# Optimization experiments

Hardware: AMD Instinct MI355X
Metric: run time of the kernel (lower is better)

## Reference

```python
import jax, jax.numpy as jnp
import numpy as np

B, S, HIDDEN = 2, 2048, 2048
NUM_HEADS, NUM_KV_HEADS, HEAD_DIM = 16, 4, 128
Q_SIZE = NUM_HEADS * HEAD_DIM          # 2048
KV_SIZE = NUM_KV_HEADS * HEAD_DIM      # 512
ROPE_THETA = 10000.0
NEG = -1e30


def setup_inputs() -> dict:
    key = jax.random.key(0)
    k1, k2, k3 = jax.random.split(key, 3)
    hidden_states = jax.random.normal(k1, (B, S, HIDDEN), jnp.float32)
    w_qkv = jax.random.normal(k2, (HIDDEN, Q_SIZE + 2 * KV_SIZE), jnp.float32) / np.sqrt(HIDDEN)
    w_o = jax.random.normal(k3, (Q_SIZE, HIDDEN), jnp.float32) / np.sqrt(Q_SIZE)
    positions = jnp.broadcast_to(jnp.arange(S, dtype=jnp.int32), (B, S))
    return {"positions": positions, "hidden_states": hidden_states,
            "w_qkv": w_qkv, "w_o": w_o}


def _rope(x, positions):
    # x: [B, S, H, D], neox-style rotate-half rope over full head_dim
    d = x.shape[-1]
    inv_freq = 1.0 / (ROPE_THETA ** (jnp.arange(0, d, 2, dtype=jnp.float32) / d))
    ang = positions[..., None].astype(jnp.float32) * inv_freq      # [B, S, D/2]
    cos = jnp.cos(ang)[:, :, None, :]
    sin = jnp.sin(ang)[:, :, None, :]
    x1, x2 = jnp.split(x, 2, axis=-1)
    return jnp.concatenate([x1 * cos - x2 * sin, x2 * cos + x1 * sin], axis=-1)


def reference(positions, hidden_states, w_qkv, w_o):
    qkv = jnp.einsum('bsh,ho->bso', hidden_states, w_qkv)
    q, k, v = jnp.split(qkv, [Q_SIZE, Q_SIZE + KV_SIZE], axis=-1)
    q = q.reshape(B, S, NUM_HEADS, HEAD_DIM)
    k = k.reshape(B, S, NUM_KV_HEADS, HEAD_DIM)
    v = v.reshape(B, S, NUM_KV_HEADS, HEAD_DIM)
    q = _rope(q, positions)
    k = _rope(k, positions)
    rep = NUM_HEADS // NUM_KV_HEADS
    k = jnp.repeat(k, rep, axis=2)   # GQA expand -> [B, S, NUM_HEADS, D]
    v = jnp.repeat(v, rep, axis=2)
    scale = HEAD_DIM ** -0.5
    scores = jnp.einsum('bqhd,bkhd->bhqk', q, k) * scale   # [B, H, S, S]
    causal = jnp.tril(jnp.ones((S, S), dtype=bool))
    scores = jnp.where(causal, scores, NEG)
    probs = jax.nn.softmax(scores, axis=-1)
    attn = jnp.einsum('bhqk,bkhd->bqhd', probs, v).reshape(B, S, Q_SIZE)
    return jnp.einsum('bsq,qh->bsh', attn, w_o)
```

## Files before the change

kernel.cpp:

```cpp
#include <hip/hip_runtime.h>
#include <hip/hip_bf16.h>
#include <stdint.h>

#define BDIM 2
#define SDIM 2048
#define HID 2048
#define NH 16
#define NKV 4
#define HD 128
#define QSZ 2048
#define KVSZ 512
#define QKVW 3072
#define TOK (BDIM*SDIM)

typedef __attribute__((ext_vector_type(8))) short bf16x8;
typedef __attribute__((ext_vector_type(4))) float f32x4;
typedef __attribute__((ext_vector_type(16))) float f32x16;

__device__ __forceinline__ short f2bf(float f) {
  return (short)__bfloat16_as_ushort(__float2bfloat16(f));
}

__device__ __forceinline__ float exp2_fast(float x) {
  float r;
  asm("v_exp_f32 %0, %1" : "=v"(r) : "v"(x));
  return r;
}

__device__ __forceinline__ void gload_lds16(const void* g, void* lds) {
  __builtin_amdgcn_global_load_lds(
      (const __attribute__((address_space(1))) void*)g,
      (__attribute__((address_space(3))) void*)lds, 16, 0, 0);
}

__global__ __launch_bounds__(256) void k_cvt_bf16(const float* __restrict__ in,
                                                  short* __restrict__ out, int n) {
  int i = (blockIdx.x * 256 + threadIdx.x) * 4;
  if (i >= n) return;
  float4 v = *(const float4*)(in + i);
  short4 o; o.x = f2bf(v.x); o.y = f2bf(v.y); o.z = f2bf(v.z); o.w = f2bf(v.w);
  *(short4*)(out + i) = o;
}

__global__ __launch_bounds__(256) void k_transpose_cvt(const float* __restrict__ in,
                                                       short* __restrict__ out,
                                                       int R, int C) {
  __shared__ short tile[64][65];
  int k0 = blockIdx.y * 64;
  int n0 = blockIdx.x * 64;
  int t = threadIdx.x;
#pragma unroll
  for (int i = 0; i < 16; ++i) {
    int idx = i * 256 + t;
    int kk = idx >> 6, nn = idx & 63;
    tile[kk][nn] = f2bf(in[(size_t)(k0 + kk) * C + n0 + nn]);
  }
  __syncthreads();
#pragma unroll
  for (int i = 0; i < 16; ++i) {
    int idx = i * 256 + t;
    int nn = idx >> 6, kk = idx & 63;
    out[(size_t)(n0 + nn) * R + k0 + kk] = tile[kk][nn];
  }
}

__global__ __launch_bounds__(256) void k_gemm_bf16(const short* __restrict__ A,
                                                   const short* __restrict__ Bt,
                                                   float* __restrict__ C,
                                                   int M, int N, int K) {
  __shared__ char lds[128 * 32 * 2 * 2];
  char* As = lds;
  char* Bs = lds + 8192;
  const int tid = threadIdx.x;
  const int w = tid >> 6, l = tid & 63;
  const int lq = l & 15, g = l >> 4;
  const int m0 = blockIdx.y * 128, n0 = blockIdx.x * 128;
  const int wm = (w >> 1) * 64, wn = (w & 1) * 64;
  f32x4 acc[4][4] = {};

  const int nk = K >> 5;
  for (int kt = 0; kt < nk; ++kt) {
    const int k0 = kt * 32;
#pragma unroll
    for (int i = 0; i < 2; ++i) {
      int ch = (w + 4 * i) * 64 + l;
      int r = ch >> 2, cc = ch & 3;
      int gc = cc ^ ((r >> 1) & 3);
      gload_lds16(A + (size_t)(m0 + r) * K + k0 + gc * 8, As + (w + 4 * i) * 1024);
      gload_lds16(Bt + (size_t)(n0 + r) * K + k0 + gc * 8, Bs + (w + 4 * i) * 1024);
    }
    __syncthreads();
    bf16x8 af[4], bfr[4];
#pragma unroll
    for (int mi = 0; mi < 4; ++mi) {
      int row = wm + mi * 16 + lq;
      af[mi] = *(const bf16x8*)(As + row * 64 + ((g ^ ((row >> 1) & 3)) * 16));
    }
#pragma unroll
    for (int ni = 0; ni < 4; ++ni) {
      int row = wn + ni * 16 + lq;
      bfr[ni] = *(const bf16x8*)(Bs + row * 64 + ((g ^ ((row >> 1) & 3)) * 16));
    }
#pragma unroll
    for (int mi = 0; mi < 4; ++mi)
#pragma unroll
      for (int ni = 0; ni < 4; ++ni)
        acc[mi][ni] = __builtin_amdgcn_mfma_f32_16x16x32_bf16(af[mi], bfr[ni],
                                                              acc[mi][ni], 0, 0, 0);
    __syncthreads();
  }
#pragma unroll
  for (int mi = 0; mi < 4; ++mi)
#pragma unroll
    for (int ni = 0; ni < 4; ++ni)
#pragma unroll
      for (int r = 0; r < 4; ++r) {
        int row = m0 + wm + mi * 16 + 4 * g + r;
        int col = n0 + wn + ni * 16 + lq;
        C[(size_t)row * N + col] = acc[mi][ni][r];
      }
}

__global__ __launch_bounds__(256) void k_gemm_qkv_rope(const short* __restrict__ A,
                                                       const short* __restrict__ Bt,
                                                       const int* __restrict__ pos,
                                                       short* __restrict__ Qh,
                                                       short* __restrict__ Kh,
                                                       short* __restrict__ VT) {
  __shared__ char lds[128 * 32 * 2 * 2];
  char* As = lds;
  char* Bs = lds + 8192;
  const int tid = threadIdx.x;
  const int w = tid >> 6, l = tid & 63;
  const int lq = l & 15, g = l >> 4;
  const int m0 = blockIdx.y * 128, n0 = blockIdx.x * 128;
  const int K = HID, N = QKVW;
  f32x4 acc[2][8] = {};

  const int nk = K >> 5;
  for (int kt = 0; kt < nk; ++kt) {
    const int k0 = kt * 32;
#pragma unroll
    for (int i = 0; i < 2; ++i) {
      int ch = (w + 4 * i) * 64 + l;
      int r = ch >> 2, cc = ch & 3;
      int gc = cc ^ ((r >> 1) & 3);
      gload_lds16(A + (size_t)(m0 + r) * K + k0 + gc * 8, As + (w + 4 * i) * 1024);
      gload_lds16(Bt + (size_t)(n0 + r) * K + k0 + gc * 8, Bs + (w + 4 * i) * 1024);
    }
    __syncthreads();
    bf16x8 af[2], bfr[8];
#pragma unroll
    for (int mi = 0; mi < 2; ++mi) {
      int row = w * 32 + mi * 16 + lq;
      af[mi] = *(const bf16x8*)(As + row * 64 + ((g ^ ((row >> 1) & 3)) * 16));
    }
#pragma unroll
    for (int ni = 0; ni < 8; ++ni) {
      int row = ni * 16 + lq;
      bfr[ni] = *(const bf16x8*)(Bs + row * 64 + ((g ^ ((row >> 1) & 3)) * 16));
    }
#pragma unroll
    for (int mi = 0; mi < 2; ++mi)
#pragma unroll
      for (int ni = 0; ni < 8; ++ni)
        acc[mi][ni] = __builtin_amdgcn_mfma_f32_16x16x32_bf16(af[mi], bfr[ni],
                                                              acc[mi][ni], 0, 0, 0);
    __syncthreads();
  }

  const int hx = blockIdx.x;
  const int b = m0 >> 11;
  if (hx < 20) {
    const float qscale = 0.12751743920f;
    const float sc = (hx < 16) ? qscale : 1.0f;
    short* dst = (hx < 16) ? (Qh + (size_t)(b * NH + hx) * SDIM * HD)
                           : (Kh + (size_t)(b * NKV + (hx - 16)) * SDIM * HD);
    float invf[4];
#pragma unroll
    for (int ni = 0; ni < 4; ++ni)
      invf[ni] = expf(-(float)(ni * 16 + lq) * (9.210340371976184f / 64.0f));
#pragma unroll
    for (int mi = 0; mi < 2; ++mi)
#pragma unroll
      for (int r = 0; r < 4; ++r) {
        int row = m0 + w * 32 + mi * 16 + 4 * g + r;
        int s = row & (SDIM - 1);
        float p = (float)pos[row];
        size_t hb = (size_t)s * HD;
#pragma unroll
        for (int ni = 0; ni < 4; ++ni) {
          float sn, cs;
          sincosf(p * invf[ni], &sn, &cs);
          float x1 = acc[mi][ni][r], x2 = acc[mi][ni + 4][r];
          dst[hb + ni * 16 + lq] = f2bf((x1 * cs - x2 * sn) * sc);
          dst[hb + ni * 16 + lq + 64] = f2bf((x2 * cs + x1 * sn) * sc);
        }
      }
  } else {
    const int hv = hx - 20;
    const int s00 = (m0 & (SDIM - 1)) + w * 32;
#pragma unroll
    for (int mi = 0; mi < 2; ++mi)
#pragma unroll
      for (int ni = 0; ni < 8; ++ni) {
        int d = ni * 16 + lq;
        int s0 = s00 + mi * 16 + 4 * g;
        size_t vb = ((size_t)(b * NKV + hv) * HD + d) * SDIM + s0;
        short4 ov;
        ov.x = f2bf(acc[mi][ni][0]); ov.y = f2bf(acc[mi][ni][1]);
        ov.z = f2bf(acc[mi][ni][2]); ov.w = f2bf(acc[mi][ni][3]);
        *(short4*)(VT + vb) = ov;
      }
  }
}

__global__ __launch_bounds__(256, 3) void k_attn(const short* __restrict__ Qh,
                                                 const short* __restrict__ Kh,
                                                 const short* __restrict__ VT,
                                                 short* __restrict__ attn, int S) {
  __shared__ char lds[2][16384];
  const int tid = threadIdx.x;
  const int w = tid >> 6, l = tid & 63;
  const int l31 = l & 31, hi = l >> 5;
  const int nqc = S / 128;
  const int bid = blockIdx.x;
  const int b = bid / (NH * nqc);
  const int rem = bid % (NH * nqc);
  const int h = rem / nqc;
  const int qc = nqc - 1 - (rem % nqc);
  const int q0 = qc * 128 + w * 32;
  const int kvh = h >> 2;
  const short* Qp = Qh + (size_t)(b * NH + h) * S * HD;
  const short* Kp = Kh + (size_t)(b * NKV + kvh) * S * HD;
  const short* Vp = VT + (size_t)(b * NKV + kvh) * HD * S;

  bf16x8 qf[8];
#pragma unroll
  for (int kc = 0; kc < 8; ++kc)
    qf[kc] = *(const bf16x8*)(Qp + (size_t)(q0 + l31) * HD + kc * 16 + hi * 8);

  f32x16 o[4] = {};
  float mrun = -1e30f, lrun = 0.f;
  const int qabs = q0 + l31;
  const int ntu = qc * 4 + 4;

#define STAGE(bufi, c0_)                                                          \
  {                                                                               \
    char* Kb = lds[bufi];                                                         \
    char* Vb = lds[bufi] + 8192;                                                  \
    _Pragma("unroll")                                                             \
    for (int i = 0; i < 2; ++i) {                                                 \
      int id = (i * 4 + w) * 64 + l;                                              \
      int kr = id >> 4, c16 = id & 15;                                            \
      gload_lds16(Kp + (size_t)((c0_) + kr) * HD + ((c16 ^ (kr & 7)) * 8),        \
                  Kb + (i * 4 + w) * 1024);                                       \
      int vr = id >> 2, c4 = id & 3;                                              \
      gload_lds16(Vp + (size_t)vr * S + (c0_) + ((c4 ^ ((vr >> 1) & 3)) * 8),     \
                  Vb + (i * 4 + w) * 1024);                                       \
    }                                                                             \
  }

  STAGE(0, 0);
  asm volatile("s_waitcnt vmcnt(0)" ::: "memory");
  __builtin_amdgcn_s_barrier();

  for (int c = 0; c < ntu; ++c) {
    const int c0 = c * 32;
    const int cur = c & 1;
    if (c + 1 < ntu) STAGE(cur ^ 1, c0 + 32);
    const char* Ks = lds[cur];
    const char* Vs = lds[cur] + 8192;

    f32x16 st = {};
    __builtin_amdgcn_s_setprio(1);
#pragma unroll
    for (int kc = 0; kc < 8; ++kc) {
      bf16x8 kf = *(const bf16x8*)(Ks + l31 * 256 + (((kc * 2 + hi) ^ (l31 & 7)) * 16));
      st = __builtin_amdgcn_mfma_f32_32x32x16_bf16(kf, qf[kc], st, 0, 0, 0);
    }
    __builtin_amdgcn_s_setprio(0);
    float tmax = -1e30f;
#pragma unroll
    for (int r = 0; r < 16; ++r) {
      int kv = c0 + (r & 3) + 8 * (r >> 2) + 4 * hi;
      float sv = (kv <= qabs) ? st[r] : -1e30f;
      st[r] = sv;
      tmax = fmaxf(tmax, sv);
    }
    tmax = fmaxf(tmax, __shfl_xor(tmax, 32));
    if (!__all(tmax - mrun <= 8.0f)) {
      float mnew = fmaxf(mrun, tmax);
      float fac = exp2_fast(mrun - mnew);
      lrun *= fac;
#pragma unroll
      for (int d0 = 0; d0 < 4; ++d0) o[d0] = o[d0] * fac;
      mrun = mnew;
    }
    float sum = 0.f;
#pragma unroll
    for (int r = 0; r < 16; ++r) {
      float e = exp2_fast(st[r] - mrun);
      st[r] = e;
      sum += e;
    }
    sum += __shfl_xor(sum, 32);
    lrun += sum;
    __builtin_amdgcn_s_setprio(1);
#pragma unroll
    for (int j = 0; j < 2; ++j) {
      uint32_t W0 = (uint32_t)(uint16_t)f2bf(st[8 * j + 0]) |
                    ((uint32_t)(uint16_t)f2bf(st[8 * j + 1]) << 16);
      uint32_t W1 = (uint32_t)(uint16_t)f2bf(st[8 * j + 2]) |
                    ((uint32_t)(uint16_t)f2bf(st[8 * j + 3]) << 16);
      uint32_t W2 = (uint32_t)(uint16_t)f2bf(st[8 * j + 4]) |
                    ((uint32_t)(uint16_t)f2bf(st[8 * j + 5]) << 16);
      uint32_t W3 = (uint32_t)(uint16_t)f2bf(st[8 * j + 6]) |
                    ((uint32_t)(uint16_t)f2bf(st[8 * j + 7]) << 16);
      uint32_t Y0 = __shfl_xor(hi ? W0 : W2, 32);
      uint32_t Y1 = __shfl_xor(hi ? W1 : W3, 32);
      union { uint32_t u[4]; bf16x8 v; } pu;
      pu.u[0] = hi ? Y0 : W0;
      pu.u[1] = hi ? Y1 : W1;
      pu.u[2] = hi ? W2 : Y0;
      pu.u[3] = hi ? W3 : Y1;
#pragma unroll
      for (int d0 = 0; d0 < 4; ++d0) {
        int vr = d0 * 32 + l31;
        bf16x8 vf = *(const bf16x8*)(Vs + vr * 64 + (((j * 2 + hi) ^ ((vr >> 1) & 3)) * 16));
        o[d0] = __builtin_amdgcn_mfma_f32_32x32x16_bf16(vf, pu.v, o[d0], 0, 0, 0);
      }
    }
    __builtin_amdgcn_s_setprio(0);
    asm volatile("s_waitcnt vmcnt(0)" ::: "memory");
    __builtin_amdgcn_s_barrier();
  }
#undef STAGE
  float inv = 1.0f / lrun;
  size_t rowb = (size_t)(b * S + q0 + l31) * QSZ + h * HD;
#pragma unroll
  for (int d0 = 0; d0 < 4; ++d0)
#pragma unroll
    for (int gq = 0; gq < 4; ++gq) {
      short4 ov;
      ov.x = f2bf(o[d0][4 * gq + 0] * inv);
      ov.y = f2bf(o[d0][4 * gq + 1] * inv);
      ov.z = f2bf(o[d0][4 * gq + 2] * inv);
      ov.w = f2bf(o[d0][4 * gq + 3] * inv);
      *(short4*)(attn + rowb + d0 * 32 + 8 * gq + 4 * hi) = ov;
    }
}

extern "C" void kernel_launch(void* const* d_in, const int* in_sizes, int n_in,
                              void* d_out, int out_size, void* d_ws, size_t ws_size,
                              hipStream_t stream) {
  const int* positions = (const int*)d_in[0];
  const float* hidden = (const float*)d_in[1];
  const float* w_qkv = (const float*)d_in[2];
  const float* w_o = (const float*)d_in[3];
  float* out = (float*)d_out;

  char* ws = (char*)d_ws;
  short* X     = (short*)(ws);
  short* WqkvT = (short*)(ws + 16777216);
  short* WoT   = (short*)(ws + 29360128);
  short* Qh    = (short*)(ws + 88080384);
  short* Kh    = (short*)(ws + 104857600);
  short* VT    = (short*)(ws + 109051904);
  short* ATT   = (short*)(ws + 113246208);

  k_cvt_bf16<<<8192, 256, 0, stream>>>(hidden, X, TOK * HID);
  k_transpose_cvt<<<dim3(QKVW / 64, HID / 64), 256, 0, stream>>>(w_qkv, WqkvT, HID, QKVW);
  k_transpose_cvt<<<dim3(HID / 64, QSZ / 64), 256, 0, stream>>>(w_o, WoT, QSZ, HID);
  k_gemm_qkv_rope<<<dim3(QKVW / 128, TOK / 128), 256, 0, stream>>>(X, WqkvT, positions,
                                                                   Qh, Kh, VT);
  k_attn<<<BDIM * NH * (SDIM / 128), 256, 0, stream>>>(Qh, Kh, VT, ATT, SDIM);
  k_gemm_bf16<<<dim3(HID / 128, TOK / 128), 256, 0, stream>>>(ATT, WoT, out, TOK, HID, QSZ);
}
```

Before: 238.6 us.

## Split attention KV range into two halves with separate combine kernel

The attention kernel now splits each query block's causal KV range into two equal halves, each handled by its own workgroup. Each half writes a partial normalized output and its row max and sum, and a new combine kernel merges the two partials into the final attention tensor. The aim is to double the grid and even out the causal load imbalance across CUs. The cost is an extra kernel launch, extra global traffic for the partial outputs, and a second bf16 rounding of the partials. The change also widens the K LDS swizzle to 16 and raises the launch-bounds occupancy hint to 4.

```diff
diff --git a/kernel.cpp b/kernel.cpp
--- a/kernel.cpp
+++ b/kernel.cpp
@@ -19,6 +19,9 @@
 
 __device__ __forceinline__ short f2bf(float f) {
   return (short)__bfloat16_as_ushort(__float2bfloat16(f));
+}
+__device__ __forceinline__ float bf2f(short s) {
+  return __uint_as_float(((uint32_t)(uint16_t)s) << 16);
 }
 
 __device__ __forceinline__ float exp2_fast(float x) {
@@ -134,7 +137,7 @@
   const int w = tid >> 6, l = tid & 63;
   const int lq = l & 15, g = l >> 4;
   const int m0 = blockIdx.y * 128, n0 = blockIdx.x * 128;
-  const int K = HID, N = QKVW;
+  const int K = HID;
   f32x4 acc[2][8] = {};
 
   const int nk = K >> 5;
@@ -215,18 +218,22 @@
   }
 }
 
-__global__ __launch_bounds__(256, 3) void k_attn(const short* __restrict__ Qh,
+__global__ __launch_bounds__(256, 4) void k_attn(const short* __restrict__ Qh,
                                                  const short* __restrict__ Kh,
                                                  const short* __restrict__ VT,
-                                                 short* __restrict__ attn, int S) {
+                                                 short* __restrict__ Op,
+                                                 float* __restrict__ ml, int S) {
   __shared__ char lds[2][16384];
   const int tid = threadIdx.x;
   const int w = tid >> 6, l = tid & 63;
   const int l31 = l & 31, hi = l >> 5;
   const int nqc = S / 128;
+  const int per = BDIM * NH * nqc;
   const int bid = blockIdx.x;
-  const int b = bid / (NH * nqc);
-  const int rem = bid % (NH * nqc);
+  const int sp = bid / per;
+  const int rem2 = bid % per;
+  const int b = rem2 / (NH * nqc);
+  const int rem = rem2 % (NH * nqc);
   const int h = rem / nqc;
   const int qc = nqc - 1 - (rem % nqc);
   const int q0 = qc * 128 + w * 32;
@@ -243,7 +250,8 @@
   f32x16 o[4] = {};
   float mrun = -1e30f, lrun = 0.f;
   const int qabs = q0 + l31;
-  const int ntu = qc * 4 + 4;
+  const int nspl = 2 * qc + 2;
+  const int cs = sp * nspl, ce = cs + nspl;
 
 #define STAGE(bufi, c0_)                                                          \
   {                                                                               \
@@ -253,7 +261,7 @@
     for (int i = 0; i < 2; ++i) {                                                 \
       int id = (i * 4 + w) * 64 + l;                                              \
       int kr = id >> 4, c16 = id & 15;                                            \
-      gload_lds16(Kp + (size_t)((c0_) + kr) * HD + ((c16 ^ (kr & 7)) * 8),        \
+      gload_lds16(Kp + (size_t)((c0_) + kr) * HD + ((c16 ^ (kr & 15)) * 8),       \
                   Kb + (i * 4 + w) * 1024);                                       \
       int vr = id >> 2, c4 = id & 3;                                              \
       gload_lds16(Vp + (size_t)vr * S + (c0_) + ((c4 ^ ((vr >> 1) & 3)) * 8),     \
@@ -261,14 +269,14 @@
     }                                                                             \
   }
 
-  STAGE(0, 0);
+  STAGE(cs & 1, cs * 32);
   asm volatile("s_waitcnt vmcnt(0)" ::: "memory");
   __builtin_amdgcn_s_barrier();
 
-  for (int c = 0; c < ntu; ++c) {
+  for (int c = cs; c < ce; ++c) {
     const int c0 = c * 32;
     const int cur = c & 1;
-    if (c + 1 < ntu) STAGE(cur ^ 1, c0 + 32);
+    if (c + 1 < ce) STAGE(cur ^ 1, c0 + 32);
     const char* Ks = lds[cur];
     const char* Vs = lds[cur] + 8192;
 
@@ -276,7 +284,7 @@
     __builtin_amdgcn_s_setprio(1);
 #pragma unroll
     for (int kc = 0; kc < 8; ++kc) {
-      bf16x8 kf = *(const bf16x8*)(Ks + l31 * 256 + (((kc * 2 + hi) ^ (l31 & 7)) * 16));
+      bf16x8 kf = *(const bf16x8*)(Ks + l31 * 256 + (((kc * 2 + hi) ^ (l31 & 15)) * 16));
       st = __builtin_amdgcn_mfma_f32_32x32x16_bf16(kf, qf[kc], st, 0, 0, 0);
     }
     __builtin_amdgcn_s_setprio(0);
@@ -336,7 +344,8 @@
     __builtin_amdgcn_s_barrier();
   }
 #undef STAGE
-  float inv = 1.0f / lrun;
+  float inv = (lrun > 0.f) ? 1.0f / lrun : 0.f;
+  short* Od = Op + (size_t)sp * TOK * QSZ;
   size_t rowb = (size_t)(b * S + q0 + l31) * QSZ + h * HD;
 #pragma unroll
   for (int d0 = 0; d0 < 4; ++d0)
@@ -347,8 +356,38 @@
       ov.y = f2bf(o[d0][4 * gq + 1] * inv);
       ov.z = f2bf(o[d0][4 * gq + 2] * inv);
       ov.w = f2bf(o[d0][4 * gq + 3] * inv);
-      *(short4*)(attn + rowb + d0 * 32 + 8 * gq + 4 * hi) = ov;
-    }
+      *(short4*)(Od + rowb + d0 * 32 + 8 * gq + 4 * hi) = ov;
+    }
+  if (hi == 0) {
+    float2 t; t.x = mrun; t.y = lrun;
+    *(float2*)(ml + (((size_t)sp * BDIM + b) * NH + h) * S * 2 + (size_t)(q0 + l31) * 2) = t;
+  }
+}
+
+__global__ __launch_bounds__(256) void k_combine(const short* __restrict__ Op,
+                                                 const float* __restrict__ ml,
+                                                 short* __restrict__ attn) {
+  int idx = blockIdx.x * 256 + threadIdx.x;
+  int row = idx >> 8;
+  int col8 = (idx & 255) * 8;
+  int h = col8 >> 7;
+  int b = row >> 11, q = row & (SDIM - 1);
+  size_t mlbase = (((size_t)b * NH + h) * SDIM + q) * 2;
+  float2 m1 = *(const float2*)(ml + mlbase);
+  float2 m2 = *(const float2*)(ml + mlbase + (size_t)BDIM * NH * SDIM * 2);
+  float M = fmaxf(m1.x, m2.x);
+  float w1 = m1.y * exp2_fast(m1.x - M);
+  float w2 = m2.y * exp2_fast(m2.x - M);
+  float rr = 1.0f / (w1 + w2);
+  float r1 = w1 * rr, r2 = w2 * rr;
+  size_t off = (size_t)row * QSZ + col8;
+  bf16x8 a = *(const bf16x8*)(Op + off);
+  bf16x8 c = *(const bf16x8*)(Op + (size_t)TOK * QSZ + off);
+  short ov[8];
+#pragma unroll
+  for (int j = 0; j < 8; ++j)
+    ov[j] = f2bf(r1 * bf2f(a[j]) + r2 * bf2f(c[j]));
+  *(bf16x8*)(attn + off) = *(bf16x8*)ov;
 }
 
 extern "C" void kernel_launch(void* const* d_in, const int* in_sizes, int n_in,
@@ -364,6 +403,8 @@
   short* X     = (short*)(ws);
   short* WqkvT = (short*)(ws + 16777216);
   short* WoT   = (short*)(ws + 29360128);
+  short* Op    = (short*)(ws + 37748736);
+  float* ml    = (float*)(ws + 71303168);
   short* Qh    = (short*)(ws + 88080384);
   short* Kh    = (short*)(ws + 104857600);
   short* VT    = (short*)(ws + 109051904);
@@ -374,6 +415,7 @@
   k_transpose_cvt<<<dim3(HID / 64, QSZ / 64), 256, 0, stream>>>(w_o, WoT, QSZ, HID);
   k_gemm_qkv_rope<<<dim3(QKVW / 128, TOK / 128), 256, 0, stream>>>(X, WqkvT, positions,
                                                                    Qh, Kh, VT);
-  k_attn<<<BDIM * NH * (SDIM / 128), 256, 0, stream>>>(Qh, Kh, VT, ATT, SDIM);
+  k_attn<<<2 * BDIM * NH * (SDIM / 128), 256, 0, stream>>>(Qh, Kh, VT, Op, ml, SDIM);
+  k_combine<<<TOK * QSZ / 8 / 256, 256, 0, stream>>>(Op, ml, ATT);
   k_gemm_bf16<<<dim3(HID / 128, TOK / 128), 256, 0, stream>>>(ATT, WoT, out, TOK, HID, QSZ);
 }
```

Measured after the change: 303.7 us. +27.3%, slower.

## Double attention KV tile to 64 keys per iteration with wider LDS buffers

Applied to the files above, without the earlier changes.

The attention kernel now stages 64 keys per iteration instead of 32, doubling the K and V LDS buffers to 32 KB each. It computes two 32x32 score tiles per step and runs four PV MFMA groups. LDS swizzles are adjusted to the new row widths, and occupancy drops from 3 to 2 blocks per CU. The aim is to halve the number of barriers, online-softmax rescale checks and loop overheads. In exchange it raises register pressure, lowers occupancy, and wastes more work on masked causal keys in the last tile.

```diff
diff --git a/kernel.cpp b/kernel.cpp
--- a/kernel.cpp
+++ b/kernel.cpp
@@ -134,7 +134,7 @@
   const int w = tid >> 6, l = tid & 63;
   const int lq = l & 15, g = l >> 4;
   const int m0 = blockIdx.y * 128, n0 = blockIdx.x * 128;
-  const int K = HID, N = QKVW;
+  const int K = HID;
   f32x4 acc[2][8] = {};
 
   const int nk = K >> 5;
@@ -215,11 +215,11 @@
   }
 }
 
-__global__ __launch_bounds__(256, 3) void k_attn(const short* __restrict__ Qh,
+__global__ __launch_bounds__(256, 2) void k_attn(const short* __restrict__ Qh,
                                                  const short* __restrict__ Kh,
                                                  const short* __restrict__ VT,
                                                  short* __restrict__ attn, int S) {
-  __shared__ char lds[2][16384];
+  __shared__ char lds[2][32768];
   const int tid = threadIdx.x;
   const int w = tid >> 6, l = tid & 63;
   const int l31 = l & 31, hi = l >> 5;
@@ -243,20 +243,20 @@
   f32x16 o[4] = {};
   float mrun = -1e30f, lrun = 0.f;
   const int qabs = q0 + l31;
-  const int ntu = qc * 4 + 4;
+  const int ntu = qc * 2 + 2;
 
 #define STAGE(bufi, c0_)                                                          \
   {                                                                               \
     char* Kb = lds[bufi];                                                         \
-    char* Vb = lds[bufi] + 8192;                                                  \
+    char* Vb = lds[bufi] + 16384;                                                 \
     _Pragma("unroll")                                                             \
-    for (int i = 0; i < 2; ++i) {                                                 \
+    for (int i = 0; i < 4; ++i) {                                                 \
       int id = (i * 4 + w) * 64 + l;                                              \
       int kr = id >> 4, c16 = id & 15;                                            \
-      gload_lds16(Kp + (size_t)((c0_) + kr) * HD + ((c16 ^ (kr & 7)) * 8),        \
+      gload_lds16(Kp + (size_t)((c0_) + kr) * HD + ((c16 ^ (kr & 15)) * 8),       \
                   Kb + (i * 4 + w) * 1024);                                       \
-      int vr = id >> 2, c4 = id & 3;                                              \
-      gload_lds16(Vp + (size_t)vr * S + (c0_) + ((c4 ^ ((vr >> 1) & 3)) * 8),     \
+      int vr = id >> 3, c8 = id & 7;                                              \
+      gload_lds16(Vp + (size_t)vr * S + (c0_) + ((c8 ^ (vr & 7)) * 8),            \
                   Vb + (i * 4 + w) * 1024);                                       \
     }                                                                             \
   }
@@ -266,28 +266,36 @@
   __builtin_amdgcn_s_barrier();
 
   for (int c = 0; c < ntu; ++c) {
-    const int c0 = c * 32;
+    const int c0 = c * 64;
     const int cur = c & 1;
-    if (c + 1 < ntu) STAGE(cur ^ 1, c0 + 32);
+    if (c + 1 < ntu) STAGE(cur ^ 1, c0 + 64);
     const char* Ks = lds[cur];
-    const char* Vs = lds[cur] + 8192;
-
-    f32x16 st = {};
+    const char* Vs = lds[cur] + 16384;
+
+    f32x16 st[2];
     __builtin_amdgcn_s_setprio(1);
 #pragma unroll
-    for (int kc = 0; kc < 8; ++kc) {
-      bf16x8 kf = *(const bf16x8*)(Ks + l31 * 256 + (((kc * 2 + hi) ^ (l31 & 7)) * 16));
-      st = __builtin_amdgcn_mfma_f32_32x32x16_bf16(kf, qf[kc], st, 0, 0, 0);
+    for (int tt = 0; tt < 2; ++tt) {
+      f32x16 s = {};
+#pragma unroll
+      for (int kc = 0; kc < 8; ++kc) {
+        int kr = tt * 32 + l31;
+        bf16x8 kf = *(const bf16x8*)(Ks + kr * 256 + (((kc * 2 + hi) ^ (l31 & 15)) * 16));
+        s = __builtin_amdgcn_mfma_f32_32x32x16_bf16(kf, qf[kc], s, 0, 0, 0);
+      }
+      st[tt] = s;
     }
     __builtin_amdgcn_s_setprio(0);
     float tmax = -1e30f;
 #pragma unroll
-    for (int r = 0; r < 16; ++r) {
-      int kv = c0 + (r & 3) + 8 * (r >> 2) + 4 * hi;
-      float sv = (kv <= qabs) ? st[r] : -1e30f;
-      st[r] = sv;
-      tmax = fmaxf(tmax, sv);
-    }
+    for (int tt = 0; tt < 2; ++tt)
+#pragma unroll
+      for (int r = 0; r < 16; ++r) {
+        int kv = c0 + tt * 32 + (r & 3) + 8 * (r >> 2) + 4 * hi;
+        float sv = (kv <= qabs) ? st[tt][r] : -1e30f;
+        st[tt][r] = sv;
+        tmax = fmaxf(tmax, sv);
+      }
     tmax = fmaxf(tmax, __shfl_xor(tmax, 32));
     if (!__all(tmax - mrun <= 8.0f)) {
       float mnew = fmaxf(mrun, tmax);
@@ -299,24 +307,27 @@
     }
     float sum = 0.f;
 #pragma unroll
-    for (int r = 0; r < 16; ++r) {
-      float e = exp2_fast(st[r] - mrun);
-      st[r] = e;
-      sum += e;
-    }
+    for (int tt = 0; tt < 2; ++tt)
+#pragma unroll
+      for (int r = 0; r < 16; ++r) {
+        float e = exp2_fast(st[tt][r] - mrun);
+        st[tt][r] = e;
+        sum += e;
+      }
     sum += __shfl_xor(sum, 32);
     lrun += sum;
     __builtin_amdgcn_s_setprio(1);
 #pragma unroll
-    for (int j = 0; j < 2; ++j) {
-      uint32_t W0 = (uint32_t)(uint16_t)f2bf(st[8 * j + 0]) |
-                    ((uint32_t)(uint16_t)f2bf(st[8 * j + 1]) << 16);
-      uint32_t W1 = (uint32_t)(uint16_t)f2bf(st[8 * j + 2]) |
-                    ((uint32_t)(uint16_t)f2bf(st[8 * j + 3]) << 16);
-      uint32_t W2 = (uint32_t)(uint16_t)f2bf(st[8 * j + 4]) |
-                    ((uint32_t)(uint16_t)f2bf(st[8 * j + 5]) << 16);
-      uint32_t W3 = (uint32_t)(uint16_t)f2bf(st[8 * j + 6]) |
-                    ((uint32_t)(uint16_t)f2bf(st[8 * j + 7]) << 16);
+    for (int j = 0; j < 4; ++j) {
+      const int tt = j >> 1, kc = j & 1;
+      uint32_t W0 = (uint32_t)(uint16_t)f2bf(st[tt][8 * kc + 0]) |
+                    ((uint32_t)(uint16_t)f2bf(st[tt][8 * kc + 1]) << 16);
+      uint32_t W1 = (uint32_t)(uint16_t)f2bf(st[tt][8 * kc + 2]) |
+                    ((uint32_t)(uint16_t)f2bf(st[tt][8 * kc + 3]) << 16);
+      uint32_t W2 = (uint32_t)(uint16_t)f2bf(st[tt][8 * kc + 4]) |
+                    ((uint32_t)(uint16_t)f2bf(st[tt][8 * kc + 5]) << 16);
+      uint32_t W3 = (uint32_t)(uint16_t)f2bf(st[tt][8 * kc + 6]) |
+                    ((uint32_t)(uint16_t)f2bf(st[tt][8 * kc + 7]) << 16);
       uint32_t Y0 = __shfl_xor(hi ? W0 : W2, 32);
       uint32_t Y1 = __shfl_xor(hi ? W1 : W3, 32);
       union { uint32_t u[4]; bf16x8 v; } pu;
@@ -327,7 +338,7 @@
 #pragma unroll
       for (int d0 = 0; d0 < 4; ++d0) {
         int vr = d0 * 32 + l31;
-        bf16x8 vf = *(const bf16x8*)(Vs + vr * 64 + (((j * 2 + hi) ^ ((vr >> 1) & 3)) * 16));
+        bf16x8 vf = *(const bf16x8*)(Vs + vr * 128 + (((j * 2 + hi) ^ (vr & 7)) * 16));
         o[d0] = __builtin_amdgcn_mfma_f32_32x32x16_bf16(vf, pu.v, o[d0], 0, 0, 0);
       }
     }
```

Result: faster. 232.0 us (-2.8%).

## Split attention KV range across two wave groups and merge partial softmax in LDS

Applied to the files above, without the earlier changes.

The attention kernel now launches 512 threads per block. Two groups of four waves each process half of the causal KV tiles for the same 128 query rows, and their partial outputs and running max/sum are combined through LDS at the end. This shortens the serial KV loop per block and adds intra-CTA parallelism, at the cost of more LDS, a final merge step, and a bf16 round-trip of one partial result. Smaller changes also skip causal masking on fully unmasked tiles, widen the K LDS swizzle, and replace sincosf/expf in RoPE with hardware v_sin/v_cos/v_exp on revolution-scaled angles. The hardware sin/cos path may lose accuracy for large angles.

```diff
diff --git a/kernel.cpp b/kernel.cpp
--- a/kernel.cpp
+++ b/kernel.cpp
@@ -20,11 +20,22 @@
 __device__ __forceinline__ short f2bf(float f) {
   return (short)__bfloat16_as_ushort(__float2bfloat16(f));
 }
+__device__ __forceinline__ float bf2f(short s) {
+  return __uint_as_float(((uint32_t)(uint16_t)s) << 16);
+}
 
 __device__ __forceinline__ float exp2_fast(float x) {
   float r;
   asm("v_exp_f32 %0, %1" : "=v"(r) : "v"(x));
   return r;
+}
+
+__device__ __forceinline__ void sincos_rev(float rev, float* sn, float* cs) {
+  float fr, s, c;
+  asm("v_fract_f32 %0, %1" : "=v"(fr) : "v"(rev));
+  asm("v_sin_f32 %0, %1" : "=v"(s) : "v"(fr));
+  asm("v_cos_f32 %0, %1" : "=v"(c) : "v"(fr));
+  *sn = s; *cs = c;
 }
 
 __device__ __forceinline__ void gload_lds16(const void* g, void* lds) {
@@ -134,7 +145,7 @@
   const int w = tid >> 6, l = tid & 63;
   const int lq = l & 15, g = l >> 4;
   const int m0 = blockIdx.y * 128, n0 = blockIdx.x * 128;
-  const int K = HID, N = QKVW;
+  const int K = HID;
   f32x4 acc[2][8] = {};
 
   const int nk = K >> 5;
@@ -179,7 +190,8 @@
     float invf[4];
 #pragma unroll
     for (int ni = 0; ni < 4; ++ni)
-      invf[ni] = expf(-(float)(ni * 16 + lq) * (9.210340371976184f / 64.0f));
+      invf[ni] = 0.15915494309f *
+                 exp2_fast(-(float)(ni * 16 + lq) * (13.287712379549449f / 64.0f));
 #pragma unroll
     for (int mi = 0; mi < 2; ++mi)
 #pragma unroll
@@ -191,7 +203,7 @@
 #pragma unroll
         for (int ni = 0; ni < 4; ++ni) {
           float sn, cs;
-          sincosf(p * invf[ni], &sn, &cs);
+          sincos_rev(p * invf[ni], &sn, &cs);
           float x1 = acc[mi][ni][r], x2 = acc[mi][ni + 4][r];
           dst[hb + ni * 16 + lq] = f2bf((x1 * cs - x2 * sn) * sc);
           dst[hb + ni * 16 + lq + 64] = f2bf((x2 * cs + x1 * sn) * sc);
@@ -215,25 +227,28 @@
   }
 }
 
-__global__ __launch_bounds__(256, 3) void k_attn(const short* __restrict__ Qh,
+__global__ __launch_bounds__(512, 4) void k_attn(const short* __restrict__ Qh,
                                                  const short* __restrict__ Kh,
                                                  const short* __restrict__ VT,
                                                  short* __restrict__ attn, int S) {
-  __shared__ char lds[2][16384];
+  __shared__ char lds[65536];
   const int tid = threadIdx.x;
   const int w = tid >> 6, l = tid & 63;
   const int l31 = l & 31, hi = l >> 5;
+  const int wq = w & 3;
+  const int sp = w >> 2;
   const int nqc = S / 128;
   const int bid = blockIdx.x;
   const int b = bid / (NH * nqc);
   const int rem = bid % (NH * nqc);
   const int h = rem / nqc;
   const int qc = nqc - 1 - (rem % nqc);
-  const int q0 = qc * 128 + w * 32;
+  const int q0 = qc * 128 + wq * 32;
   const int kvh = h >> 2;
   const short* Qp = Qh + (size_t)(b * NH + h) * S * HD;
   const short* Kp = Kh + (size_t)(b * NKV + kvh) * S * HD;
   const short* Vp = VT + (size_t)(b * NKV + kvh) * HD * S;
+  char* base = lds + sp * 32768;
 
   bf16x8 qf[8];
 #pragma unroll
@@ -243,50 +258,56 @@
   f32x16 o[4] = {};
   float mrun = -1e30f, lrun = 0.f;
   const int qabs = q0 + l31;
-  const int ntu = qc * 4 + 4;
+  const int halfT = qc * 2 + 2;
+  const int cbeg = sp * halfT;
 
 #define STAGE(bufi, c0_)                                                          \
   {                                                                               \
-    char* Kb = lds[bufi];                                                         \
-    char* Vb = lds[bufi] + 8192;                                                  \
+    char* Kb = base + (bufi) * 16384;                                             \
+    char* Vb = Kb + 8192;                                                         \
     _Pragma("unroll")                                                             \
     for (int i = 0; i < 2; ++i) {                                                 \
-      int id = (i * 4 + w) * 64 + l;                                              \
+      int id = (i * 4 + wq) * 64 + l;                                             \
       int kr = id >> 4, c16 = id & 15;                                            \
-      gload_lds16(Kp + (size_t)((c0_) + kr) * HD + ((c16 ^ (kr & 7)) * 8),        \
-                  Kb + (i * 4 + w) * 1024);                                       \
+      gload_lds16(Kp + (size_t)((c0_) + kr) * HD + ((c16 ^ (kr & 15)) * 8),       \
+                  Kb + (i * 4 + wq) * 1024);                                      \
       int vr = id >> 2, c4 = id & 3;                                              \
       gload_lds16(Vp + (size_t)vr * S + (c0_) + ((c4 ^ ((vr >> 1) & 3)) * 8),     \
-                  Vb + (i * 4 + w) * 1024);                                       \
+                  Vb + (i * 4 + wq) * 1024);                                      \
     }                                                                             \
   }
 
-  STAGE(0, 0);
+  STAGE(0, cbeg * 32);
   asm volatile("s_waitcnt vmcnt(0)" ::: "memory");
   __builtin_amdgcn_s_barrier();
 
-  for (int c = 0; c < ntu; ++c) {
-    const int c0 = c * 32;
-    const int cur = c & 1;
-    if (c + 1 < ntu) STAGE(cur ^ 1, c0 + 32);
-    const char* Ks = lds[cur];
-    const char* Vs = lds[cur] + 8192;
+  for (int t = 0; t < halfT; ++t) {
+    const int c0 = (cbeg + t) * 32;
+    const int cur = t & 1;
+    if (t + 1 < halfT) STAGE(cur ^ 1, c0 + 32);
+    const char* Ks = base + cur * 16384;
+    const char* Vs = Ks + 8192;
 
     f32x16 st = {};
     __builtin_amdgcn_s_setprio(1);
 #pragma unroll
     for (int kc = 0; kc < 8; ++kc) {
-      bf16x8 kf = *(const bf16x8*)(Ks + l31 * 256 + (((kc * 2 + hi) ^ (l31 & 7)) * 16));
+      bf16x8 kf = *(const bf16x8*)(Ks + l31 * 256 + (((kc * 2 + hi) ^ (l31 & 15)) * 16));
       st = __builtin_amdgcn_mfma_f32_32x32x16_bf16(kf, qf[kc], st, 0, 0, 0);
     }
     __builtin_amdgcn_s_setprio(0);
     float tmax = -1e30f;
-#pragma unroll
-    for (int r = 0; r < 16; ++r) {
-      int kv = c0 + (r & 3) + 8 * (r >> 2) + 4 * hi;
-      float sv = (kv <= qabs) ? st[r] : -1e30f;
-      st[r] = sv;
-      tmax = fmaxf(tmax, sv);
+    if (c0 + 32 <= q0) {
+#pragma unroll
+      for (int r = 0; r < 16; ++r) tmax = fmaxf(tmax, st[r]);
+    } else {
+#pragma unroll
+      for (int r = 0; r < 16; ++r) {
+        int kv = c0 + (r & 3) + 8 * (r >> 2) + 4 * hi;
+        float sv = (kv <= qabs) ? st[r] : -1e30f;
+        st[r] = sv;
+        tmax = fmaxf(tmax, sv);
+      }
     }
     tmax = fmaxf(tmax, __shfl_xor(tmax, 32));
     if (!__all(tmax - mrun <= 8.0f)) {
@@ -336,19 +357,46 @@
     __builtin_amdgcn_s_barrier();
   }
 #undef STAGE
-  float inv = 1.0f / lrun;
-  size_t rowb = (size_t)(b * S + q0 + l31) * QSZ + h * HD;
-#pragma unroll
-  for (int d0 = 0; d0 < 4; ++d0)
-#pragma unroll
-    for (int gq = 0; gq < 4; ++gq) {
-      short4 ov;
-      ov.x = f2bf(o[d0][4 * gq + 0] * inv);
-      ov.y = f2bf(o[d0][4 * gq + 1] * inv);
-      ov.z = f2bf(o[d0][4 * gq + 2] * inv);
-      ov.w = f2bf(o[d0][4 * gq + 3] * inv);
-      *(short4*)(attn + rowb + d0 * 32 + 8 * gq + 4 * hi) = ov;
-    }
+
+  if (sp == 1) {
+    char* ob = lds + wq * 9216 + l * 144;
+#pragma unroll
+    for (int d0 = 0; d0 < 4; ++d0)
+#pragma unroll
+      for (int gh = 0; gh < 2; ++gh) {
+        short t8[8];
+#pragma unroll
+        for (int j = 0; j < 8; ++j) t8[j] = f2bf(o[d0][gh * 8 + j]);
+        *(bf16x8*)(ob + (d0 * 2 + gh) * 16) = *(bf16x8*)t8;
+      }
+    if (hi == 0) {
+      float2 t; t.x = mrun; t.y = lrun;
+      *(float2*)(lds + 40960 + wq * 256 + l31 * 8) = t;
+    }
+  }
+  __syncthreads();
+  if (sp == 0) {
+    float2 m2 = *(const float2*)(lds + 40960 + wq * 256 + l31 * 8);
+    float M = fmaxf(mrun, m2.x);
+    float a1 = exp2_fast(mrun - M), a2 = exp2_fast(m2.x - M);
+    float denom = lrun * a1 + m2.y * a2;
+    float f1 = a1 / denom, f2v = a2 / denom;
+    const char* ob = lds + wq * 9216 + l * 144;
+    size_t rowb = (size_t)(b * S + q0 + l31) * QSZ + h * HD;
+#pragma unroll
+    for (int d0 = 0; d0 < 4; ++d0)
+#pragma unroll
+      for (int gq = 0; gq < 4; ++gq) {
+        bf16x8 v2 = *(const bf16x8*)(ob + (d0 * 2 + (gq >> 1)) * 16);
+        int e0 = (gq & 1) * 4;
+        short4 ov;
+        ov.x = f2bf(o[d0][4 * gq + 0] * f1 + bf2f(v2[e0 + 0]) * f2v);
+        ov.y = f2bf(o[d0][4 * gq + 1] * f1 + bf2f(v2[e0 + 1]) * f2v);
+        ov.z = f2bf(o[d0][4 * gq + 2] * f1 + bf2f(v2[e0 + 2]) * f2v);
+        ov.w = f2bf(o[d0][4 * gq + 3] * f1 + bf2f(v2[e0 + 3]) * f2v);
+        *(short4*)(attn + rowb + d0 * 32 + 8 * gq + 4 * hi) = ov;
+      }
+  }
 }
 
 extern "C" void kernel_launch(void* const* d_in, const int* in_sizes, int n_in,
@@ -374,6 +422,6 @@
   k_transpose_cvt<<<dim3(HID / 64, QSZ / 64), 256, 0, stream>>>(w_o, WoT, QSZ, HID);
   k_gemm_qkv_rope<<<dim3(QKVW / 128, TOK / 128), 256, 0, stream>>>(X, WqkvT, positions,
                                                                    Qh, Kh, VT);
-  k_attn<<<BDIM * NH * (SDIM / 128), 256, 0, stream>>>(Qh, Kh, VT, ATT, SDIM);
+  k_attn<<<BDIM * NH * (SDIM / 128), 512, 0, stream>>>(Qh, Kh, VT, ATT, SDIM);
   k_gemm_bf16<<<dim3(HID / 128, TOK / 128), 256, 0, stream>>>(ATT, WoT, out, TOK, HID, QSZ);
 }
```

Result: slower. 283.8 us (+18.9%).
